# Kernel tuning notes

Measured on AMD Instinct MI355X. Metric: run time of the kernel, lower is better.

Reference implementation:

```python
import jax, jax.numpy as jnp
import numpy as np

N_HEAD = 16
N_FEAT = 1024
D_K = N_FEAT // N_HEAD


def rtt_half(x):
    x1, x2 = x[..., : x.shape[-1] // 2], x[..., x.shape[-1] // 2 :]
    return jnp.concatenate([-x2, x1], axis=-1)


def setup_inputs() -> dict:
    key = jax.random.key(0)
    ks = jax.random.split(key, 16)
    B, T, D = 4, 2048, N_FEAT
    inp = {
        "query": jax.random.normal(ks[0], (B, T, D), jnp.float32),
        "key": jax.random.normal(ks[1], (B, T, D), jnp.float32),
        "value": jax.random.normal(ks[2], (B, T, D), jnp.float32),
        "cos": jax.random.uniform(ks[3], (T, 1, D_K), jnp.float32),
        "sin": jax.random.uniform(ks[4], (T, 1, D_K), jnp.float32),
        "mask": jnp.zeros((B, T, T), jnp.bool_),
    }
    s = 1.0 / np.sqrt(D)
    inp["Wq"] = jax.random.uniform(ks[5], (D, D), jnp.float32, -s, s)
    inp["bq"] = jax.random.uniform(ks[6], (D,), jnp.float32, -s, s)
    inp["Wk"] = jax.random.uniform(ks[7], (D, D), jnp.float32, -s, s)
    inp["bk"] = jax.random.uniform(ks[8], (D,), jnp.float32, -s, s)
    inp["Wv"] = jax.random.uniform(ks[9], (D, D), jnp.float32, -s, s)
    inp["bv"] = jax.random.uniform(ks[10], (D,), jnp.float32, -s, s)
    inp["Wo"] = jax.random.uniform(ks[11], (D, D), jnp.float32, -s, s)
    inp["bo"] = jax.random.uniform(ks[12], (D,), jnp.float32, -s, s)
    return inp


def reference(query, key, value, cos, sin, mask, Wq, bq, Wk, bk, Wv, bv, Wo, bo):
    B, T, D = query.shape
    h, d_k = N_HEAD, D_K
    # QKV projections (torch Linear: x @ W.T + b), reshape to (B,T,h,d_k)
    q = (query @ Wq.T + bq).reshape(B, T, h, d_k)
    k = (key @ Wk.T + bk).reshape(B, T, h, d_k)
    v = (value @ Wv.T + bv).reshape(B, T, h, d_k)
    # RoPE: cos/sin sliced to T, broadcast (T,1,d_k) over (B,T,h,d_k)
    c, s = cos[:T], sin[:T]
    q = q * c + rtt_half(q) * s
    k = k * c + rtt_half(k) * s
    # attention scores (B,h,T,T)
    scores = jnp.einsum("bqhd,bkhd->bhqk", q, k) / np.sqrt(d_k).astype(jnp.float32)
    scores = jnp.where(mask[:, None, :, :], -jnp.inf, scores)
    attn = jax.nn.softmax(scores, axis=-1)
    out = jnp.einsum("bhqk,bkhd->bqhd", attn, v).reshape(B, T, D)
    return out @ Wo.T + bo
```

## Files before the change

### kernel.cpp

```cpp
#include <hip/hip_runtime.h>

#define B_SZ 4
#define T_SZ 2048
#define D_SZ 1024
#define H_SZ 16
#define DK_SZ 64
#define M_SZ (B_SZ * T_SZ)

typedef __attribute__((ext_vector_type(8))) short bf16x8;
typedef __attribute__((ext_vector_type(4))) float f32x4;

union fui { float f; unsigned u; };

static __device__ inline short f2bf(float x) {
    union { float f; unsigned u; } v; v.f = x;
    unsigned r = v.u + 0x7fff + ((v.u >> 16) & 1);
    return (short)(r >> 16);
}
static __device__ inline void split1(float f, short* h, short* l) {
    fui a; a.f = f;
    *h = (short)(a.u >> 16);
    fui t; t.u = a.u & 0xffff0000u;
    fui r; r.f = f - t.f;
    *l = (short)(r.u >> 16);
}

#define MFMA16(a, b, c) __builtin_amdgcn_mfma_f32_16x16x32_bf16((a), (b), (c), 0, 0, 0)

#define GLDS16(g, l) __builtin_amdgcn_global_load_lds(                        \
    (const __attribute__((address_space(1))) unsigned int*)(g),               \
    (__attribute__((address_space(3))) unsigned int*)(l), 16, 0, 0)

static __device__ inline void split4_store(const float4 f, short4* Hp, short4* Lp)
{
    fui a[4]; a[0].f = f.x; a[1].f = f.y; a[2].f = f.z; a[3].f = f.w;
    union { short s[4]; short4 v; } H, L;
#pragma unroll
    for (int j = 0; j < 4; ++j) {
        H.s[j] = (short)(a[j].u >> 16);
        fui t; t.u = a[j].u & 0xffff0000u;
        fui r; r.f = a[j].f - t.f;
        L.s[j] = (short)(r.u >> 16);
    }
    *Hp = H.v; *Lp = L.v;
}

__global__ __launch_bounds__(256)
void wsplit_kernel(const float* __restrict__ W, short* __restrict__ Wh,
                   short* __restrict__ Wl)
{
    const size_t i = (size_t)blockIdx.x * 256 + threadIdx.x;
    split4_store(((const float4*)W)[i], &((short4*)Wh)[i], &((short4*)Wl)[i]);
}

__global__ __launch_bounds__(256)
void preproc_kernel(const float* __restrict__ W0, const float* __restrict__ W1,
                    const float* __restrict__ W2, const float* __restrict__ W3,
                    const float* __restrict__ query,
                    short* __restrict__ Whd, short* __restrict__ Wld,
                    short* __restrict__ Xh, short* __restrict__ Xl,
                    const unsigned char* __restrict__ mask, int* __restrict__ flags)
{
    const int bid = blockIdx.x;
    const int tid = threadIdx.x;
    if (bid < 4096) {
        const int which = bid >> 10;
        const float* W = (which == 0) ? W0 : (which == 1) ? W1 : (which == 2) ? W2 : W3;
        const size_t i = (size_t)(bid & 1023) * 256 + tid;
        short* Hd = Whd + (size_t)which * 2 * D_SZ * D_SZ;
        short* Ld = Wld + (size_t)which * 2 * D_SZ * D_SZ;
        split4_store(((const float4*)W)[i], &((short4*)Hd)[i], &((short4*)Ld)[i]);
    } else if (bid < 12288) {
        const size_t i = (size_t)(bid - 4096) * 256 + tid;
        split4_store(((const float4*)query)[i], &((short4*)Xh)[i], &((short4*)Xl)[i]);
    } else {
        const int f = (bid - 12288) * 4 + (tid >> 6);
        const int lane = tid & 63;
        const int b = f >> 10, qt = (f >> 5) & 31, kt = f & 31;
        const unsigned char* base = mask + ((size_t)b * T_SZ + qt * 64) * T_SZ + kt * 64;
        bool nz = false;
#pragma unroll
        for (int i2 = 0; i2 < 4; ++i2) {
            const int c = lane + 64 * i2;
            const int row = c >> 2, off = (c & 3) * 16;
            uint4 v = *(const uint4*)(base + (size_t)row * T_SZ + off);
            nz |= ((v.x | v.y | v.z | v.w) != 0);
        }
        unsigned long long bal = __ballot(nz);
        if (lane == 0) flags[f] = (bal != 0) ? 1 : 0;
    }
}

__global__ __launch_bounds__(256)
void qkv_mfma_kernel(const short* __restrict__ Ah, const short* __restrict__ Al,
                     const short* __restrict__ Wh, const short* __restrict__ Wl,
                     const float* __restrict__ bias,
                     const float* __restrict__ cosb, const float* __restrict__ sinb,
                     short* __restrict__ Hd, short* __restrict__ Ld,
                     short* __restrict__ Vb, const int which)
{
    __shared__ __align__(16) short Ahs[2][4096];
    __shared__ __align__(16) short Als[2][4096];
    __shared__ __align__(16) short Whs[2][4096];
    __shared__ __align__(16) short Wls[2][4096];

    const int m0 = blockIdx.x * 128, n0 = blockIdx.y * 128;
    const int tid = threadIdx.x;
    const int wv = tid >> 6, lane = tid & 63;
    const int wm = wv >> 1, wn = wv & 1;
    const int l15 = lane & 15, quad = lane >> 4;

    f32x4 acc[4][4];
#pragma unroll
    for (int mt = 0; mt < 4; ++mt)
#pragma unroll
        for (int nt = 0; nt < 4; ++nt)
            acc[mt][nt] = (f32x4){0.f, 0.f, 0.f, 0.f};

    const size_t aoff = (size_t)(m0 + wv * 32 + (lane >> 2)) * D_SZ + (lane & 3) * 8;
    const size_t woff = (size_t)(n0 + wv * 32 + (lane >> 2)) * D_SZ + (lane & 3) * 8;
    const short* ahg = Ah + aoff;
    const short* alg = Al + aoff;
    const short* whg = Wh + woff;
    const short* wlg = Wl + woff;

#define STAGEQ(bi, kk)                                                        \
    do {                                                                      \
        short* a0 = &Ahs[bi][wv * 1024];                                      \
        short* a1 = &Als[bi][wv * 1024];                                      \
        short* w0 = &Whs[bi][wv * 1024];                                      \
        short* w1 = &Wls[bi][wv * 1024];                                      \
        GLDS16(ahg + (kk),             a0);                                   \
        GLDS16(ahg + 16 * D_SZ + (kk), a0 + 512);                             \
        GLDS16(alg + (kk),             a1);                                   \
        GLDS16(alg + 16 * D_SZ + (kk), a1 + 512);                             \
        GLDS16(whg + (kk),             w0);                                   \
        GLDS16(whg + 16 * D_SZ + (kk), w0 + 512);                             \
        GLDS16(wlg + (kk),             w1);                                   \
        GLDS16(wlg + 16 * D_SZ + (kk), w1 + 512);                             \
    } while (0)

    STAGEQ(0, 0);
    for (int k0 = 0; k0 < D_SZ; k0 += 32) {
        const int cur = (k0 >> 5) & 1;
        __syncthreads();
        if (k0 + 32 < D_SZ) STAGEQ(cur ^ 1, k0 + 32);

        bf16x8 ah[4], al[4];
#pragma unroll
        for (int mt = 0; mt < 4; ++mt) {
            const int arow = (wm * 64 + mt * 16 + l15) * 32 + quad * 8;
            ah[mt] = *(const bf16x8*)&Ahs[cur][arow];
            al[mt] = *(const bf16x8*)&Als[cur][arow];
        }
#pragma unroll
        for (int nt = 0; nt < 4; ++nt) {
            const int brow = (wn * 64 + nt * 16 + l15) * 32 + quad * 8;
            const bf16x8 bh = *(const bf16x8*)&Whs[cur][brow];
            const bf16x8 bl = *(const bf16x8*)&Wls[cur][brow];
#pragma unroll
            for (int mt = 0; mt < 4; ++mt) {
                acc[mt][nt] = MFMA16(ah[mt], bh, acc[mt][nt]);
                acc[mt][nt] = MFMA16(al[mt], bh, acc[mt][nt]);
                acc[mt][nt] = MFMA16(ah[mt], bl, acc[mt][nt]);
            }
        }
    }
#undef STAGEQ

    const int hh = (blockIdx.y << 1) + wn;
    if (which < 2) {
        const float qscale = (which == 0) ? 0.125f : 1.0f;
#pragma unroll
        for (int mt = 0; mt < 4; ++mt)
#pragma unroll
            for (int p = 0; p < 2; ++p) {
                const int d1 = p * 16 + l15, d2 = d1 + 32;
                const int col1 = n0 + wn * 64 + d1;
                const float b1 = bias[col1], b2 = bias[col1 + 32];
#pragma unroll
                for (int r = 0; r < 4; ++r) {
                    const int m = m0 + wm * 64 + mt * 16 + quad * 4 + r;
                    const int bb = m >> 11, tg = m & (T_SZ - 1);
                    const float c1 = cosb[tg * 64 + d1], s1 = sinb[tg * 64 + d1];
                    const float c2 = cosb[tg * 64 + d2], s2 = sinb[tg * 64 + d2];
                    const float x1 = acc[mt][p][r] + b1;
                    const float x2 = acc[mt][p + 2][r] + b2;
                    const float y1 = (x1 * c1 - x2 * s1) * qscale;
                    const float y2 = (x2 * c2 + x1 * s2) * qscale;
                    const size_t base = (((size_t)(bb * H_SZ + hh)) * T_SZ + tg) * 64;
                    short h_, l_;
                    split1(y1, &h_, &l_); Hd[base + d1] = h_; Ld[base + d1] = l_;
                    split1(y2, &h_, &l_); Hd[base + d2] = h_; Ld[base + d2] = l_;
                }
            }
    } else {
#pragma unroll
        for (int nt = 0; nt < 4; ++nt) {
            const int d = nt * 16 + l15;
            const float bvv = bias[n0 + wn * 64 + d];
#pragma unroll
            for (int mt = 0; mt < 4; ++mt)
#pragma unroll
                for (int r = 0; r < 4; ++r) {
                    const int m = m0 + wm * 64 + mt * 16 + quad * 4 + r;
                    const int bb = m >> 11, tg = m & (T_SZ - 1);
                    Vb[(((size_t)(bb * H_SZ + hh)) * T_SZ + tg) * 64 + d] =
                        f2bf(acc[mt][nt][r] + bvv);
                }
        }
    }
}

__global__ __launch_bounds__(256)
void gemm_out_kernel(const short* __restrict__ Ah, const short* __restrict__ Al,
                     const short* __restrict__ Wh, const short* __restrict__ Wl,
                     const float* __restrict__ bias, float* __restrict__ C)
{
    __shared__ __align__(16) short Ahs[2][4096];
    __shared__ __align__(16) short Als[2][4096];
    __shared__ __align__(16) short Whs[2][4096];
    __shared__ __align__(16) short Wls[2][4096];

    const int m0 = blockIdx.x * 128, n0 = blockIdx.y * 128;
    const int tid = threadIdx.x;
    const int wv = tid >> 6, lane = tid & 63;
    const int wm = wv >> 1, wn = wv & 1;
    const int l15 = lane & 15, quad = lane >> 4;

    f32x4 acc[4][4];
#pragma unroll
    for (int mt = 0; mt < 4; ++mt)
#pragma unroll
        for (int nt = 0; nt < 4; ++nt)
            acc[mt][nt] = (f32x4){0.f, 0.f, 0.f, 0.f};

    const size_t aoff = (size_t)(m0 + wv * 32 + (lane >> 2)) * D_SZ + (lane & 3) * 8;
    const size_t woff = (size_t)(n0 + wv * 32 + (lane >> 2)) * D_SZ + (lane & 3) * 8;
    const short* ahg = Ah + aoff;
    const short* alg = Al + aoff;
    const short* whg = Wh + woff;
    const short* wlg = Wl + woff;

#define STAGEO(bi, kk)                                                        \
    do {                                                                      \
        short* a0 = &Ahs[bi][wv * 1024];                                      \
        short* a1 = &Als[bi][wv * 1024];                                      \
        short* w0 = &Whs[bi][wv * 1024];                                      \
        short* w1 = &Wls[bi][wv * 1024];                                      \
        GLDS16(ahg + (kk),             a0);                                   \
        GLDS16(ahg + 16 * D_SZ + (kk), a0 + 512);                             \
        GLDS16(alg + (kk),             a1);                                   \
        GLDS16(alg + 16 * D_SZ + (kk), a1 + 512);                             \
        GLDS16(whg + (kk),             w0);                                   \
        GLDS16(whg + 16 * D_SZ + (kk), w0 + 512);                             \
        GLDS16(wlg + (kk),             w1);                                   \
        GLDS16(wlg + 16 * D_SZ + (kk), w1 + 512);                             \
    } while (0)

    STAGEO(0, 0);
    for (int k0 = 0; k0 < D_SZ; k0 += 32) {
        const int cur = (k0 >> 5) & 1;
        __syncthreads();
        if (k0 + 32 < D_SZ) STAGEO(cur ^ 1, k0 + 32);

        bf16x8 ah[4], al[4];
#pragma unroll
        for (int mt = 0; mt < 4; ++mt) {
            const int arow = (wm * 64 + mt * 16 + l15) * 32 + quad * 8;
            ah[mt] = *(const bf16x8*)&Ahs[cur][arow];
            al[mt] = *(const bf16x8*)&Als[cur][arow];
        }
#pragma unroll
        for (int nt = 0; nt < 4; ++nt) {
            const int brow = (wn * 64 + nt * 16 + l15) * 32 + quad * 8;
            const bf16x8 bh = *(const bf16x8*)&Whs[cur][brow];
            const bf16x8 bl = *(const bf16x8*)&Wls[cur][brow];
#pragma unroll
            for (int mt = 0; mt < 4; ++mt) {
                acc[mt][nt] = MFMA16(ah[mt], bh, acc[mt][nt]);
                acc[mt][nt] = MFMA16(al[mt], bh, acc[mt][nt]);
                acc[mt][nt] = MFMA16(ah[mt], bl, acc[mt][nt]);
            }
        }
    }
#undef STAGEO

#pragma unroll
    for (int nt = 0; nt < 4; ++nt) {
        const int col = n0 + wn * 64 + nt * 16 + l15;
        const float bvv = bias[col];
#pragma unroll
        for (int mt = 0; mt < 4; ++mt)
#pragma unroll
            for (int r = 0; r < 4; ++r) {
                const int m = m0 + wm * 64 + mt * 16 + quad * 4 + r;
                C[(size_t)m * D_SZ + col] = acc[mt][nt][r] + bvv;
            }
    }
}

__global__ __launch_bounds__(256, 6)
void attn_mfma_kernel(const short* __restrict__ Qhg, const short* __restrict__ Qlg,
                      const short* __restrict__ Khg, const short* __restrict__ Klg,
                      const short* __restrict__ Vg,
                      const unsigned char* __restrict__ mask,
                      const int* __restrict__ flags,
                      short* __restrict__ Oh, short* __restrict__ Ol)
{
    __shared__ __align__(16) short Khs[64 * 72];
    __shared__ __align__(16) short Kls[64 * 72];
    __shared__ __align__(16) short Vt[64 * 72];
    __shared__ __align__(16) short Ps[4 * 16 * 72];

    const int bh = blockIdx.y;
    const int b = bh >> 4, h = bh & 15;
    const int q0 = blockIdx.x * 64;
    const int tid = threadIdx.x;
    const int wv = tid >> 6, lane = tid & 63;
    const int l15 = lane & 15, quad = lane >> 4;

    const short* qhp = Qhg + ((size_t)bh * T_SZ + q0 + wv * 16 + l15) * 64 + quad * 8;
    const short* qlp = Qlg + ((size_t)bh * T_SZ + q0 + wv * 16 + l15) * 64 + quad * 8;
    bf16x8 qh[2], ql[2];
#pragma unroll
    for (int s = 0; s < 2; ++s) {
        qh[s] = *(const bf16x8*)(qhp + 32 * s);
        ql[s] = *(const bf16x8*)(qlp + 32 * s);
    }

    f32x4 accO[4];
#pragma unroll
    for (int nt = 0; nt < 4; ++nt) accO[nt] = (f32x4){0.f, 0.f, 0.f, 0.f};
    float m_i[4], l_i[4];
#pragma unroll
    for (int r = 0; r < 4; ++r) { m_i[r] = -1e30f; l_i[r] = 0.f; }

    const short* khb = Khg + (size_t)bh * T_SZ * 64;
    const short* klb = Klg + (size_t)bh * T_SZ * 64;
    const short* vb  = Vg  + (size_t)bh * T_SZ * 64;
    const unsigned char* mbase = mask + ((size_t)b * T_SZ + q0) * T_SZ;
    const int* frow = flags + ((size_t)b * 32 + blockIdx.x) * 32;

    const short* kgp[4];
    short*       kld[4];
#pragma unroll
    for (int jj = 0; jj < 4; ++jj) {
        const int cc = tid + 256 * (jj & 1);
        const int row = cc >> 3, off = (cc & 7) * 8;
        kgp[jj] = ((jj < 2) ? khb : klb) + (size_t)row * 64 + off;
        kld[jj] = ((jj < 2) ? Khs : Kls) + row * 72 + off;
    }
    const int vt0 = (tid & 15) * 4, vd0 = (tid >> 4) * 4;
    const short* vgp[4];
#pragma unroll
    for (int i = 0; i < 4; ++i)
        vgp[i] = vb + (size_t)(vt0 + i) * 64 + vd0;
    short* pw = &Ps[wv * 16 * 72];

    bf16x8 kst[4];
    uint2  rv[4];
#pragma unroll
    for (int jj = 0; jj < 4; ++jj) kst[jj] = *(const bf16x8*)(kgp[jj]);
#pragma unroll
    for (int i = 0; i < 4; ++i)    rv[i]   = *(const uint2*)(vgp[i]);

    for (int kti = 0; kti < 32; ++kti) {
        const int kt = kti * 64;
        __syncthreads();
#pragma unroll
        for (int jj = 0; jj < 4; ++jj)
            *(bf16x8*)kld[jj] = kst[jj];
#pragma unroll
        for (int c = 0; c < 4; ++c) {
            const int k = c >> 1;
            const unsigned sel = (c & 1) ? 0x07060302u : 0x05040100u;
            const unsigned lo0 = k ? rv[0].y : rv[0].x;
            const unsigned lo1 = k ? rv[1].y : rv[1].x;
            const unsigned lo2 = k ? rv[2].y : rv[2].x;
            const unsigned lo3 = k ? rv[3].y : rv[3].x;
            uint2 o;
            o.x = __builtin_amdgcn_perm(lo1, lo0, sel);
            o.y = __builtin_amdgcn_perm(lo3, lo2, sel);
            *(uint2*)&Vt[(vd0 + c) * 72 + vt0] = o;
        }
        if (kti < 31) {
            const size_t adv = (size_t)(kt + 64) * 64;
#pragma unroll
            for (int jj = 0; jj < 4; ++jj)
                kst[jj] = *(const bf16x8*)(kgp[jj] + adv);
#pragma unroll
            for (int i = 0; i < 4; ++i)
                rv[i] = *(const uint2*)(vgp[i] + adv);
        }
        __syncthreads();

        f32x4 accS[4];
        __builtin_amdgcn_s_setprio(1);
#pragma unroll
        for (int nt = 0; nt < 4; ++nt) {
            f32x4 acc = (f32x4){0.f, 0.f, 0.f, 0.f};
#pragma unroll
            for (int s = 0; s < 2; ++s) {
                const bf16x8 kh = *(const bf16x8*)&Khs[(nt * 16 + l15) * 72 + 32 * s + quad * 8];
                const bf16x8 kl = *(const bf16x8*)&Kls[(nt * 16 + l15) * 72 + 32 * s + quad * 8];
                acc = MFMA16(qh[s], kh, acc);
                acc = MFMA16(ql[s], kh, acc);
                acc = MFMA16(qh[s], kl, acc);
            }
            accS[nt] = acc;
        }
        __builtin_amdgcn_s_setprio(0);

        float sv[4][4];
        if (frow[kti]) {
#pragma unroll
            for (int nt = 0; nt < 4; ++nt)
#pragma unroll
                for (int r = 0; r < 4; ++r) {
                    const unsigned char mb =
                        mbase[(size_t)(wv * 16 + quad * 4 + r) * T_SZ + kt + nt * 16 + l15];
                    sv[nt][r] = mb ? -1e30f : accS[nt][r];
                }
        } else {
#pragma unroll
            for (int nt = 0; nt < 4; ++nt)
#pragma unroll
                for (int r = 0; r < 4; ++r)
                    sv[nt][r] = accS[nt][r];
        }

        float rmax[4];
#pragma unroll
        for (int r = 0; r < 4; ++r)
            rmax[r] = fmaxf(fmaxf(sv[0][r], sv[1][r]), fmaxf(sv[2][r], sv[3][r]));
#pragma unroll
        for (int off = 1; off < 16; off <<= 1)
#pragma unroll
            for (int r = 0; r < 4; ++r)
                rmax[r] = fmaxf(rmax[r], __shfl_xor(rmax[r], off, 64));

        float alpha[4];
#pragma unroll
        for (int r = 0; r < 4; ++r) {
            const float mnew = fmaxf(m_i[r], rmax[r]);
            alpha[r] = __expf(m_i[r] - mnew);
            m_i[r] = mnew;
        }
        float lsum[4] = {0.f, 0.f, 0.f, 0.f};
#pragma unroll
        for (int nt = 0; nt < 4; ++nt)
#pragma unroll
            for (int r = 0; r < 4; ++r) {
                const float p = __expf(sv[nt][r] - m_i[r]);
                sv[nt][r] = p;
                lsum[r] += p;
            }
#pragma unroll
        for (int r = 0; r < 4; ++r)
            l_i[r] = l_i[r] * alpha[r] + lsum[r];

#pragma unroll
        for (int nt = 0; nt < 4; ++nt)
#pragma unroll
            for (int r = 0; r < 4; ++r) {
                fui u; u.f = sv[nt][r];
                pw[(quad * 4 + r) * 72 + nt * 16 + l15] = (short)((u.u + 0x8000u) >> 16);
            }

#pragma unroll
        for (int nt = 0; nt < 4; ++nt)
#pragma unroll
            for (int r = 0; r < 4; ++r)
                accO[nt][r] *= alpha[r];

        bf16x8 pa[2];
#pragma unroll
        for (int s = 0; s < 2; ++s)
            pa[s] = *(const bf16x8*)&pw[l15 * 72 + 32 * s + quad * 8];
        __builtin_amdgcn_s_setprio(1);
#pragma unroll
        for (int nt = 0; nt < 4; ++nt)
#pragma unroll
            for (int s = 0; s < 2; ++s) {
                const bf16x8 vf = *(const bf16x8*)&Vt[(nt * 16 + l15) * 72 + 32 * s + quad * 8];
                accO[nt] = MFMA16(pa[s], vf, accO[nt]);
            }
        __builtin_amdgcn_s_setprio(0);
    }

#pragma unroll
    for (int off = 1; off < 16; off <<= 1)
#pragma unroll
        for (int r = 0; r < 4; ++r)
            l_i[r] += __shfl_xor(l_i[r], off, 64);

#pragma unroll
    for (int r = 0; r < 4; ++r) {
        const float inv = 1.f / l_i[r];
        const int t = q0 + wv * 16 + quad * 4 + r;
        const size_t base = ((size_t)(b * T_SZ + t)) * D_SZ + h * DK_SZ;
#pragma unroll
        for (int nt = 0; nt < 4; ++nt) {
            short h_, l_;
            split1(accO[nt][r] * inv, &h_, &l_);
            Oh[base + nt * 16 + l15] = h_;
            Ol[base + nt * 16 + l15] = l_;
        }
    }
}

extern "C" void kernel_launch(void* const* d_in, const int* in_sizes, int n_in,
                              void* d_out, int out_size, void* d_ws, size_t ws_size,
                              hipStream_t stream)
{
    const float* query = (const float*)d_in[0];
    const float* key   = (const float*)d_in[1];
    const float* value = (const float*)d_in[2];
    const float* cosb  = (const float*)d_in[3];
    const float* sinb  = (const float*)d_in[4];
    const unsigned char* mask = (const unsigned char*)d_in[5];
    const float* Wq = (const float*)d_in[6];
    const float* bq = (const float*)d_in[7];
    const float* Wk = (const float*)d_in[8];
    const float* bk = (const float*)d_in[9];
    const float* Wv = (const float*)d_in[10];
    const float* bv = (const float*)d_in[11];
    const float* Wo = (const float*)d_in[12];
    const float* bo = (const float*)d_in[13];
    float* out = (float*)d_out;

    short* sp = (short*)d_ws;
    const size_t eb = (size_t)B_SZ * H_SZ * T_SZ * DK_SZ;
    short* Qh = sp;          short* Ql = sp + eb;
    short* Kh = sp + 2 * eb; short* Kl = sp + 3 * eb;
    short* Vb = sp + 4 * eb;
    short* Xh = sp + 5 * eb; short* Xl = sp + 6 * eb;
    short* wsp = sp + 7 * eb;
    const size_t wlen = (size_t)D_SZ * D_SZ;
    short* wqh = wsp;            short* wql = wsp + wlen;
    short* wkh = wsp + 2 * wlen; short* wkl = wsp + 3 * wlen;
    short* wvh = wsp + 4 * wlen; short* wvl = wsp + 5 * wlen;
    short* woh = wsp + 6 * wlen; short* wol = wsp + 7 * wlen;
    int* flags = (int*)(wsp + 8 * wlen);

    const int aBlocks = (int)((size_t)M_SZ * D_SZ / 4 / 256);
    preproc_kernel<<<4096 + 8192 + 1024, 256, 0, stream>>>(
        Wq, Wk, Wv, Wo, query, wqh, wql, Xh, Xl, mask, flags);

    qkv_mfma_kernel<<<dim3(M_SZ / 128, 8), 256, 0, stream>>>(
        Xh, Xl, wqh, wql, bq, cosb, sinb, Qh, Ql, Vb, 0);
    wsplit_kernel<<<aBlocks, 256, 0, stream>>>(key, Xh, Xl);
    qkv_mfma_kernel<<<dim3(M_SZ / 128, 8), 256, 0, stream>>>(
        Xh, Xl, wkh, wkl, bk, cosb, sinb, Kh, Kl, Vb, 1);
    wsplit_kernel<<<aBlocks, 256, 0, stream>>>(value, Xh, Xl);
    qkv_mfma_kernel<<<dim3(M_SZ / 128, 8), 256, 0, stream>>>(
        Xh, Xl, wvh, wvl, bv, cosb, sinb, Qh, Ql, Vb, 2);

    attn_mfma_kernel<<<dim3(T_SZ / 64, B_SZ * H_SZ), 256, 0, stream>>>(
        Qh, Ql, Kh, Kl, Vb, mask, flags, Xh, Xl);

    gemm_out_kernel<<<dim3(M_SZ / 128, D_SZ / 128), 256, 0, stream>>>(
        Xh, Xl, woh, wol, bo, out);
}
```

Measured before the change: 670.0 us.

## Load GEMM A operand directly from global into registers, skipping LDS staging

In the QKV and output-projection GEMMs, the A-operand hi/lo tiles are no longer staged through shared memory. Each wave now reads its A fragments straight from global memory into registers every k-step, while only the weight tiles keep the double-buffered LDS path. Launch bounds are also raised to request 4 blocks per SM. This halves LDS usage per block and aims for higher occupancy, but A loads become synchronous global reads on the critical path with no prefetch. Since two waves share each A row block, those rows are also fetched redundantly from global memory or cache.

```diff
diff --git a/kernel.cpp b/kernel.cpp
--- a/kernel.cpp
+++ b/kernel.cpp
@@ -91,7 +91,7 @@
     }
 }
 
-__global__ __launch_bounds__(256)
+__global__ __launch_bounds__(256, 4)
 void qkv_mfma_kernel(const short* __restrict__ Ah, const short* __restrict__ Al,
                      const short* __restrict__ Wh, const short* __restrict__ Wl,
                      const float* __restrict__ bias,
@@ -99,8 +99,6 @@
                      short* __restrict__ Hd, short* __restrict__ Ld,
                      short* __restrict__ Vb, const int which)
 {
-    __shared__ __align__(16) short Ahs[2][4096];
-    __shared__ __align__(16) short Als[2][4096];
     __shared__ __align__(16) short Whs[2][4096];
     __shared__ __align__(16) short Wls[2][4096];
 
@@ -117,41 +115,40 @@
         for (int nt = 0; nt < 4; ++nt)
             acc[mt][nt] = (f32x4){0.f, 0.f, 0.f, 0.f};
 
-    const size_t aoff = (size_t)(m0 + wv * 32 + (lane >> 2)) * D_SZ + (lane & 3) * 8;
+    const short* aph[4];
+    const short* apl[4];
+#pragma unroll
+    for (int mt = 0; mt < 4; ++mt) {
+        const size_t ro = (size_t)(m0 + wm * 64 + mt * 16 + l15) * D_SZ + quad * 8;
+        aph[mt] = Ah + ro;
+        apl[mt] = Al + ro;
+    }
+
     const size_t woff = (size_t)(n0 + wv * 32 + (lane >> 2)) * D_SZ + (lane & 3) * 8;
-    const short* ahg = Ah + aoff;
-    const short* alg = Al + aoff;
     const short* whg = Wh + woff;
     const short* wlg = Wl + woff;
 
-#define STAGEQ(bi, kk)                                                        \
+#define STAGEW(bi, kk)                                                        \
     do {                                                                      \
-        short* a0 = &Ahs[bi][wv * 1024];                                      \
-        short* a1 = &Als[bi][wv * 1024];                                      \
         short* w0 = &Whs[bi][wv * 1024];                                      \
         short* w1 = &Wls[bi][wv * 1024];                                      \
-        GLDS16(ahg + (kk),             a0);                                   \
-        GLDS16(ahg + 16 * D_SZ + (kk), a0 + 512);                             \
-        GLDS16(alg + (kk),             a1);                                   \
-        GLDS16(alg + 16 * D_SZ + (kk), a1 + 512);                             \
         GLDS16(whg + (kk),             w0);                                   \
         GLDS16(whg + 16 * D_SZ + (kk), w0 + 512);                             \
         GLDS16(wlg + (kk),             w1);                                   \
         GLDS16(wlg + 16 * D_SZ + (kk), w1 + 512);                             \
     } while (0)
 
-    STAGEQ(0, 0);
+    STAGEW(0, 0);
     for (int k0 = 0; k0 < D_SZ; k0 += 32) {
         const int cur = (k0 >> 5) & 1;
         __syncthreads();
-        if (k0 + 32 < D_SZ) STAGEQ(cur ^ 1, k0 + 32);
+        if (k0 + 32 < D_SZ) STAGEW(cur ^ 1, k0 + 32);
 
         bf16x8 ah[4], al[4];
 #pragma unroll
         for (int mt = 0; mt < 4; ++mt) {
-            const int arow = (wm * 64 + mt * 16 + l15) * 32 + quad * 8;
-            ah[mt] = *(const bf16x8*)&Ahs[cur][arow];
-            al[mt] = *(const bf16x8*)&Als[cur][arow];
+            ah[mt] = *(const bf16x8*)(aph[mt] + k0);
+            al[mt] = *(const bf16x8*)(apl[mt] + k0);
         }
 #pragma unroll
         for (int nt = 0; nt < 4; ++nt) {
@@ -166,7 +163,7 @@
             }
         }
     }
-#undef STAGEQ
+#undef STAGEW
 
     const int hh = (blockIdx.y << 1) + wn;
     if (which < 2) {
@@ -212,13 +209,11 @@
     }
 }
 
-__global__ __launch_bounds__(256)
+__global__ __launch_bounds__(256, 4)
 void gemm_out_kernel(const short* __restrict__ Ah, const short* __restrict__ Al,
                      const short* __restrict__ Wh, const short* __restrict__ Wl,
                      const float* __restrict__ bias, float* __restrict__ C)
 {
-    __shared__ __align__(16) short Ahs[2][4096];
-    __shared__ __align__(16) short Als[2][4096];
     __shared__ __align__(16) short Whs[2][4096];
     __shared__ __align__(16) short Wls[2][4096];
 
@@ -235,41 +230,40 @@
         for (int nt = 0; nt < 4; ++nt)
             acc[mt][nt] = (f32x4){0.f, 0.f, 0.f, 0.f};
 
-    const size_t aoff = (size_t)(m0 + wv * 32 + (lane >> 2)) * D_SZ + (lane & 3) * 8;
+    const short* aph[4];
+    const short* apl[4];
+#pragma unroll
+    for (int mt = 0; mt < 4; ++mt) {
+        const size_t ro = (size_t)(m0 + wm * 64 + mt * 16 + l15) * D_SZ + quad * 8;
+        aph[mt] = Ah + ro;
+        apl[mt] = Al + ro;
+    }
+
     const size_t woff = (size_t)(n0 + wv * 32 + (lane >> 2)) * D_SZ + (lane & 3) * 8;
-    const short* ahg = Ah + aoff;
-    const short* alg = Al + aoff;
     const short* whg = Wh + woff;
     const short* wlg = Wl + woff;
 
-#define STAGEO(bi, kk)                                                        \
+#define STAGEW(bi, kk)                                                        \
     do {                                                                      \
-        short* a0 = &Ahs[bi][wv * 1024];                                      \
-        short* a1 = &Als[bi][wv * 1024];                                      \
         short* w0 = &Whs[bi][wv * 1024];                                      \
         short* w1 = &Wls[bi][wv * 1024];                                      \
-        GLDS16(ahg + (kk),             a0);                                   \
-        GLDS16(ahg + 16 * D_SZ + (kk), a0 + 512);                             \
-        GLDS16(alg + (kk),             a1);                                   \
-        GLDS16(alg + 16 * D_SZ + (kk), a1 + 512);                             \
         GLDS16(whg + (kk),             w0);                                   \
         GLDS16(whg + 16 * D_SZ + (kk), w0 + 512);                             \
         GLDS16(wlg + (kk),             w1);                                   \
         GLDS16(wlg + 16 * D_SZ + (kk), w1 + 512);                             \
     } while (0)
 
-    STAGEO(0, 0);
+    STAGEW(0, 0);
     for (int k0 = 0; k0 < D_SZ; k0 += 32) {
         const int cur = (k0 >> 5) & 1;
         __syncthreads();
-        if (k0 + 32 < D_SZ) STAGEO(cur ^ 1, k0 + 32);
+        if (k0 + 32 < D_SZ) STAGEW(cur ^ 1, k0 + 32);
 
         bf16x8 ah[4], al[4];
 #pragma unroll
         for (int mt = 0; mt < 4; ++mt) {
-            const int arow = (wm * 64 + mt * 16 + l15) * 32 + quad * 8;
-            ah[mt] = *(const bf16x8*)&Ahs[cur][arow];
-            al[mt] = *(const bf16x8*)&Als[cur][arow];
+            ah[mt] = *(const bf16x8*)(aph[mt] + k0);
+            al[mt] = *(const bf16x8*)(apl[mt] + k0);
         }
 #pragma unroll
         for (int nt = 0; nt < 4; ++nt) {
@@ -284,7 +278,7 @@
             }
         }
     }
-#undef STAGEO
+#undef STAGEW
 
 #pragma unroll
     for (int nt = 0; nt < 4; ++nt) {
```

New measurement: 868.0 us. +29.6%, slower.
